# Kernel optimization log

Measured on AMD Instinct MI355X. Metric: run time of the kernel, lower is better.

The kernel has to match this reference:

```python
import jax, jax.numpy as jnp
import numpy as np

EPS = 1e-5  # BatchNorm1d default eps


def setup_inputs() -> dict:
    key = jax.random.key(0)
    ks = jax.random.split(key, 8)
    B, N, C = 4, 4096, 512
    Ci = C // 2
    s = 1.0 / np.sqrt(C)
    si = 1.0 / np.sqrt(Ci)
    return {
        "x": jax.random.normal(ks[0], (B, N, C), jnp.float32),
        "gamma": jnp.ones((C,), jnp.float32),
        "beta": jnp.zeros((C,), jnp.float32),
        "theta_w": jax.random.normal(ks[1], (Ci, C), jnp.float32) * s,
        "theta_b": jnp.zeros((Ci,), jnp.float32),
        "phi_w": jax.random.normal(ks[2], (Ci, C), jnp.float32) * s,
        "phi_b": jnp.zeros((Ci,), jnp.float32),
        "g_w": jax.random.normal(ks[3], (Ci, C), jnp.float32) * s,
        "g_b": jnp.zeros((Ci,), jnp.float32),
        "w_w": jax.random.normal(ks[4], (C, Ci), jnp.float32) * si,
        "w_b": jnp.zeros((C,), jnp.float32),
    }


def reference(x, gamma, beta, theta_w, theta_b, phi_w, phi_b, g_w, g_b, w_w, w_b):
    # x: (B, N, C). BatchNorm1d in training mode: stats over batch and length dims.
    mean = jnp.mean(x, axis=(0, 1))                     # (C,)
    var = jnp.mean((x - mean) ** 2, axis=(0, 1))        # biased variance, (C,)
    feat = jax.nn.relu(gamma * (x - mean) * jax.lax.rsqrt(var + EPS) + beta)

    t = jnp.einsum('bnc,dc->bnd', feat, theta_w) + theta_b   # (B, N, Ci)
    p = jnp.einsum('bnc,dc->bnd', feat, phi_w) + phi_b       # (B, N, Ci)
    gx = jnp.einsum('bnc,dc->bnd', feat, g_w) + g_b          # (B, N, Ci)

    attn = jnp.einsum('bqd,bkd->bqk', t, p)             # unscaled QK^T, (B, N, N)
    attn = jax.nn.softmax(attn, axis=-1)
    y = jnp.einsum('bqk,bkd->bqd', attn, gx)            # (B, N, Ci)

    w_y = jnp.einsum('bnd,cd->bnc', y, w_w) + w_b       # (B, N, C)
    return x + w_y
```

## Files before the change

### kernel.cpp

```cpp
#include <hip/hip_runtime.h>

typedef unsigned short u16;
typedef __attribute__((ext_vector_type(4))) float f32x4;
typedef __attribute__((ext_vector_type(8))) _Float16 f16x8;
typedef __attribute__((ext_vector_type(8))) unsigned short u16x8;
typedef __attribute__((ext_vector_type(4))) unsigned short u16x4;

#define DEV __device__ __forceinline__

DEV u16 f2h(float f) {
    _Float16 h = (_Float16)f;
    u16 r;
    __builtin_memcpy(&r, &h, 2);
    return r;
}
DEV float h2f(u16 u) {
    _Float16 h;
    __builtin_memcpy(&h, &u, 2);
    return (float)h;
}

DEV f32x4 mfma16(f16x8 a, f16x8 b, f32x4 c) {
    return __builtin_amdgcn_mfma_f32_16x16x32_f16(a, b, c, 0, 0, 0);
}

DEV void gload16(const void* g, void* l) {
    __builtin_amdgcn_global_load_lds(
        (const __attribute__((address_space(1))) void*)g,
        (__attribute__((address_space(3))) void*)l, 16, 0, 0);
}

#define BB 4
#define NN 4096
#define CC 512
#define CI 256
#define RR (BB * NN)

#define OFF_FEAT 0u
#define OFF_Q    16777216u
#define OFF_K    25165824u
#define OFF_V    33554432u
#define OFF_Y    41943040u
#define OFF_WQKV 50331648u
#define OFF_WO   51118080u
#define OFF_BQKV 51380224u
#define OFF_PART 51383296u
#define OFF_SS   51907584u

__global__ void bn_partial(const float* __restrict__ x, float* __restrict__ part) {
    const int c = threadIdx.x;
    const int blk = blockIdx.x;
    const float* xp = x + (size_t)blk * 128 * CC + c;
    float s = 0.f, q = 0.f;
    for (int r = 0; r < 128; r++) {
        float v = xp[(size_t)r * CC];
        s += v; q += v * v;
    }
    part[blk * 1024 + c] = s;
    part[blk * 1024 + 512 + c] = q;
}

__global__ void bn_final(const float* __restrict__ part,
                         const float* __restrict__ gamma, const float* __restrict__ beta,
                         float* __restrict__ ss) {
    const int c = threadIdx.x;
    float s = 0.f, q = 0.f;
    for (int i = 0; i < 128; i++) {
        s += part[i * 1024 + c];
        q += part[i * 1024 + 512 + c];
    }
    float m = s * (1.0f / (float)RR);
    float var = q * (1.0f / (float)RR) - m * m;
    float istd = rsqrtf(var + 1e-5f);
    float g = gamma[c] * istd;
    ss[c] = g;
    ss[512 + c] = beta[c] - m * g;
}

__global__ void cvt_weights(const float* __restrict__ thw, const float* __restrict__ phw,
                            const float* __restrict__ gw,
                            const float* __restrict__ thb, const float* __restrict__ phb,
                            const float* __restrict__ gb,
                            const float* __restrict__ ww,
                            u16* __restrict__ wqkv, u16* __restrict__ wo,
                            float* __restrict__ bqkv) {
    const int idx = blockIdx.x * 256 + threadIdx.x;
    if (idx < 768 * 512) {
        int row = idx >> 9, col = idx & 511;
        float v = (row < 256) ? thw[row * 512 + col]
                : (row < 512) ? phw[(row - 256) * 512 + col]
                              : gw[(row - 512) * 512 + col];
        wqkv[idx] = f2h(v);
    } else if (idx < 768 * 512 + 512 * 256) {
        int j = idx - 768 * 512;
        wo[j] = f2h(ww[j]);
    }
    if (idx < 768) {
        bqkv[idx] = (idx < 256) ? thb[idx] : (idx < 512) ? phb[idx - 256] : gb[idx - 512];
    }
}

__global__ void feat_kernel(const float* __restrict__ x, const float* __restrict__ ss,
                            u16* __restrict__ feat) {
    const int total = RR * CC / 4;
    for (int idx = blockIdx.x * blockDim.x + threadIdx.x; idx < total;
         idx += gridDim.x * blockDim.x) {
        f32x4 xv = ((const f32x4*)x)[idx];
        int c4 = idx & 127;
        f32x4 sc = ((const f32x4*)ss)[c4];
        f32x4 sh = ((const f32x4*)(ss + 512))[c4];
        u16x4 o;
        #pragma unroll
        for (int e = 0; e < 4; e++) {
            float f = fmaxf(xv[e] * sc[e] + sh[e], 0.f);
            o[e] = f2h(f);
        }
        ((u16x4*)feat)[idx] = o;
    }
}

template <int MODE>
__global__ __launch_bounds__(256) void gemm_bt(
    const u16* __restrict__ A, const u16* __restrict__ Bm, int K,
    const float* __restrict__ bias, const float* __restrict__ xres,
    u16* __restrict__ oq, u16* __restrict__ okk, u16* __restrict__ ov,
    float* __restrict__ of) {
    __shared__ u16 As[128 * 32];
    __shared__ u16 Bs[128 * 32];
    const int tid = threadIdx.x;
    const int lane = tid & 63;
    const int l15 = lane & 15, kg = lane >> 4;
    const int wv = tid >> 6;
    const int wm = wv >> 1, wn = wv & 1;
    const int m0 = blockIdx.x * 128, n0 = blockIdx.y * 128;

    f32x4 acc[4][4];
    #pragma unroll
    for (int i = 0; i < 4; i++)
        #pragma unroll
        for (int j = 0; j < 4; j++) acc[i][j] = (f32x4){0.f, 0.f, 0.f, 0.f};

    const int rowA = tid >> 2, colA = (tid & 3) * 8;
    for (int k0 = 0; k0 < K; k0 += 32) {
        gload16(A + (size_t)(m0 + rowA) * K + k0 + colA, &As[tid * 8]);
        gload16(A + (size_t)(m0 + 64 + rowA) * K + k0 + colA, &As[2048 + tid * 8]);
        gload16(Bm + (size_t)(n0 + rowA) * K + k0 + colA, &Bs[tid * 8]);
        gload16(Bm + (size_t)(n0 + 64 + rowA) * K + k0 + colA, &Bs[2048 + tid * 8]);
        __syncthreads();
        f16x8 af[4], bfr[4];
        #pragma unroll
        for (int i = 0; i < 4; i++)
            af[i] = *(const f16x8*)&As[(wm * 64 + i * 16 + l15) * 32 + kg * 8];
        #pragma unroll
        for (int i = 0; i < 4; i++)
            bfr[i] = *(const f16x8*)&Bs[(wn * 64 + i * 16 + l15) * 32 + kg * 8];
        #pragma unroll
        for (int mi = 0; mi < 4; mi++)
            #pragma unroll
            for (int ni = 0; ni < 4; ni++)
                acc[mi][ni] = mfma16(af[mi], bfr[ni], acc[mi][ni]);
        __syncthreads();
    }

    #pragma unroll
    for (int mi = 0; mi < 4; mi++) {
        #pragma unroll
        for (int ni = 0; ni < 4; ni++) {
            #pragma unroll
            for (int r = 0; r < 4; r++) {
                int row = m0 + wm * 64 + mi * 16 + kg * 4 + r;
                int col = n0 + wn * 64 + ni * 16 + l15;
                float v = acc[mi][ni][r];
                if constexpr (MODE == 0) {
                    v += bias[col];
                    u16 hv = f2h(v);
                    if (n0 < 256) {
                        oq[(size_t)row * CI + col] = hv;
                    } else if (n0 < 512) {
                        okk[(size_t)row * CI + (col - 256)] = hv;
                    } else {
                        int d = col - 512;
                        int bi = row >> 12, key = row & (NN - 1);
                        int k5 = key & 31;
                        int skey = (key & ~31) |
                                   ((((k5 >> 2) & 3) << 3) | (k5 & 3) | (((k5 >> 4) & 1) << 2));
                        ov[((size_t)bi * CI + d) * NN + skey] = hv;
                    }
                } else {
                    size_t o = (size_t)row * 512 + col;
                    of[o] = xres[o] + v + bias[col];
                }
            }
        }
    }
}

#define KVB 32
#define NSPLIT 4
#define KEYS_PER (NN / NSPLIT)
#define NTILE (KEYS_PER / KVB)
#define ATTN_LDS 65536

DEV void stageK32(const u16* __restrict__ Kg, size_t kvbase, int kv0, u16* Ks, int tid) {
    const int chunk = tid & 31, rb = tid >> 5;
    #pragma unroll
    for (int i = 0; i < 4; i++) {
        int row = i * 8 + rb;
        int sc = chunk ^ (row & 7);
        gload16(Kg + kvbase + (size_t)(kv0 + row) * CI + sc * 8,
                &Ks[row * 256 + chunk * 8]);
    }
}

DEV void stageV32(const u16* __restrict__ Vtg, size_t vbase, int kv0, u16* Vt, int tid) {
    const int c = tid & 3, db = tid >> 2;
    #pragma unroll
    for (int i = 0; i < 4; i++) {
        int d = i * 64 + db;
        int sc = c ^ ((d >> 1) & 3);
        gload16(Vtg + vbase + (size_t)d * NN + kv0 + sc * 8,
                &Vt[d * KVB + c * 8]);
    }
}

__global__ __launch_bounds__(256, 2) void attn_kernel(
    const u16* __restrict__ Qg, const u16* __restrict__ Kg,
    const u16* __restrict__ Vtg, u16* __restrict__ po01, u16* __restrict__ po23,
    float* __restrict__ ml) {
    extern __shared__ u16 smem[];

    const int tid = threadIdx.x, lane = tid & 63, wv = tid >> 6;
    const int l15 = lane & 15, kg = lane >> 4;
    const int sid = (blockIdx.x & 7) * 64 + (blockIdx.x >> 3);
    const int qt = sid & 31;
    const int b = (sid >> 5) & 3;
    const int sp = sid >> 7;
    const int kvoff = sp * KEYS_PER;
    const size_t kvbase = (size_t)b * NN * CI;
    const size_t vbase = (size_t)b * CI * NN;

    f16x8 qf[2][8];
    {
        const u16* qp0 = Qg + ((size_t)b * NN + qt * 128 + wv * 32 + l15) * CI + kg * 8;
        #pragma unroll
        for (int qs = 0; qs < 2; qs++)
            #pragma unroll
            for (int kk = 0; kk < 8; kk++)
                qf[qs][kk] = *(const f16x8*)(qp0 + (size_t)qs * 16 * CI + kk * 32);
    }

    f32x4 acc[16][2];
    #pragma unroll
    for (int i = 0; i < 16; i++)
        #pragma unroll
        for (int qs = 0; qs < 2; qs++) acc[i][qs] = (f32x4){0.f, 0.f, 0.f, 0.f};
    float mrow[2] = {-1e30f, -1e30f}, lrow[2] = {0.f, 0.f};

    stageK32(Kg, kvbase, kvoff, smem, tid);
    stageV32(Vtg, vbase, kvoff, smem + 16384, tid);
    __syncthreads();

    for (int it = 0; it < NTILE; ++it) {
        const u16* Ks = smem + (it & 1) * 8192;
        const u16* Vt = smem + 16384 + (it & 1) * 8192;
        if (it + 1 < NTILE) {
            const int nxt = ((it + 1) & 1) * 8192;
            stageK32(Kg, kvbase, kvoff + (it + 1) * KVB, smem + nxt, tid);
            stageV32(Vtg, vbase, kvoff + (it + 1) * KVB, smem + 16384 + nxt, tid);
        }

        f32x4 s[2][2];
        #pragma unroll
        for (int qs = 0; qs < 2; qs++)
            #pragma unroll
            for (int nt = 0; nt < 2; nt++) s[qs][nt] = (f32x4){0.f, 0.f, 0.f, 0.f};
        __builtin_amdgcn_s_setprio(1);
        #pragma unroll
        for (int kk = 0; kk < 8; kk++) {
            #pragma unroll
            for (int nt = 0; nt < 2; nt++) {
                int krow = nt * 16 + l15;
                f16x8 kf = *(const f16x8*)&Ks[krow * 256 + (((kk * 4 + kg) ^ (krow & 7)) << 3)];
                s[0][nt] = mfma16(kf, qf[0][kk], s[0][nt]);
                s[1][nt] = mfma16(kf, qf[1][kk], s[1][nt]);
            }
        }
        __builtin_amdgcn_s_setprio(0);

        float mx[2];
        #pragma unroll
        for (int qs = 0; qs < 2; qs++) {
            float m8 = fmaxf(fmaxf(fmaxf(s[qs][0][0], s[qs][0][1]), fmaxf(s[qs][0][2], s[qs][0][3])),
                             fmaxf(fmaxf(s[qs][1][0], s[qs][1][1]), fmaxf(s[qs][1][2], s[qs][1][3])));
            m8 = fmaxf(m8, __shfl_xor(m8, 16));
            m8 = fmaxf(m8, __shfl_xor(m8, 32));
            mx[qs] = m8;
        }
        float need = fmaxf(mx[0] - mrow[0], mx[1] - mrow[1]);
        if (!__all(need <= 8.f)) {
            float sclv[2];
            #pragma unroll
            for (int qs = 0; qs < 2; qs++) {
                float mnew = fmaxf(mrow[qs], mx[qs]);
                sclv[qs] = __expf(mrow[qs] - mnew);
                lrow[qs] *= sclv[qs];
                mrow[qs] = mnew;
            }
            #pragma unroll
            for (int qs = 0; qs < 2; qs++)
                #pragma unroll
                for (int r = 0; r < 4; r++) {
                    float sr = __shfl(sclv[qs], (lane & 48) | (kg * 4 + r), 64);
                    #pragma unroll
                    for (int dt = 0; dt < 16; dt++) acc[dt][qs][r] *= sr;
                }
        }
        f16x8 pa[2];
        #pragma unroll
        for (int qs = 0; qs < 2; qs++) {
            float rs = 0.f;
            #pragma unroll
            for (int nt = 0; nt < 2; nt++)
                #pragma unroll
                for (int r = 0; r < 4; r++) {
                    float p = __expf(s[qs][nt][r] - mrow[qs]);
                    rs += p;
                    pa[qs][nt * 4 + r] = (_Float16)p;
                }
            rs += __shfl_xor(rs, 16);
            rs += __shfl_xor(rs, 32);
            lrow[qs] += rs;
        }

        __builtin_amdgcn_s_setprio(1);
        #pragma unroll
        for (int dt = 0; dt < 16; dt++) {
            int d = dt * 16 + l15;
            f16x8 vf = *(const f16x8*)&Vt[d * KVB + ((kg ^ ((l15 >> 1) & 3)) << 3)];
            acc[dt][0] = mfma16(pa[0], vf, acc[dt][0]);
            acc[dt][1] = mfma16(pa[1], vf, acc[dt][1]);
        }
        __builtin_amdgcn_s_setprio(0);

        __syncthreads();
    }

    const int row0 = b * NN + qt * 128 + wv * 32;
    u16* pod = (sp < 2) ? (po01 + (size_t)sp * RR * CI)
                        : (po23 + (size_t)(sp - 2) * RR * CI);
    #pragma unroll
    for (int qs = 0; qs < 2; qs++)
        #pragma unroll
        for (int r = 0; r < 4; r++) {
            float li = __shfl(lrow[qs], (lane & 48) | (kg * 4 + r), 64);
            float inv = 1.f / li;
            int row = row0 + qs * 16 + kg * 4 + r;
            #pragma unroll
            for (int dt = 0; dt < 16; dt++)
                pod[(size_t)row * CI + dt * 16 + l15] = f2h(acc[dt][qs][r] * inv);
        }
    if (kg == 0) {
        #pragma unroll
        for (int qs = 0; qs < 2; qs++) {
            int row = row0 + qs * 16 + l15;
            ml[row * 8 + sp * 2] = mrow[qs];
            ml[row * 8 + sp * 2 + 1] = lrow[qs];
        }
    }
}

__global__ void attn_combine(const u16* __restrict__ po01, const u16* __restrict__ po23,
                             const float* __restrict__ ml, u16* __restrict__ yb) {
    const int gid = blockIdx.x * 256 + threadIdx.x;
    const int row = gid >> 6;
    const int d0 = (gid & 63) * 4;
    f32x4 ml0 = ((const f32x4*)ml)[row * 2];
    f32x4 ml1 = ((const f32x4*)ml)[row * 2 + 1];
    float m = fmaxf(fmaxf(ml0[0], ml0[2]), fmaxf(ml1[0], ml1[2]));
    float c0 = __expf(ml0[0] - m) * ml0[1];
    float c1 = __expf(ml0[2] - m) * ml0[3];
    float c2 = __expf(ml1[0] - m) * ml1[1];
    float c3 = __expf(ml1[2] - m) * ml1[3];
    float inv = 1.f / (c0 + c1 + c2 + c3);
    u16x4 p0 = *(const u16x4*)(po01 + (size_t)row * CI + d0);
    u16x4 p1 = *(const u16x4*)(po01 + (size_t)RR * CI + (size_t)row * CI + d0);
    u16x4 p2 = *(const u16x4*)(po23 + (size_t)row * CI + d0);
    u16x4 p3 = *(const u16x4*)(po23 + (size_t)RR * CI + (size_t)row * CI + d0);
    u16x4 o;
    #pragma unroll
    for (int e = 0; e < 4; e++)
        o[e] = f2h((c0 * h2f(p0[e]) + c1 * h2f(p1[e]) +
                    c2 * h2f(p2[e]) + c3 * h2f(p3[e])) * inv);
    *(u16x4*)(yb + (size_t)row * CI + d0) = o;
}

extern "C" void kernel_launch(void* const* d_in, const int* in_sizes, int n_in,
                              void* d_out, int out_size, void* d_ws, size_t ws_size,
                              hipStream_t stream) {
    (void)in_sizes; (void)n_in; (void)out_size; (void)ws_size;
    const float* x     = (const float*)d_in[0];
    const float* gamma = (const float*)d_in[1];
    const float* beta  = (const float*)d_in[2];
    const float* thw   = (const float*)d_in[3];
    const float* thb   = (const float*)d_in[4];
    const float* phw   = (const float*)d_in[5];
    const float* phb   = (const float*)d_in[6];
    const float* gw    = (const float*)d_in[7];
    const float* gb    = (const float*)d_in[8];
    const float* ww    = (const float*)d_in[9];
    const float* wb    = (const float*)d_in[10];

    char* ws = (char*)d_ws;
    u16* feat  = (u16*)(ws + OFF_FEAT);
    u16* qb    = (u16*)(ws + OFF_Q);
    u16* kb    = (u16*)(ws + OFF_K);
    u16* vtb   = (u16*)(ws + OFF_V);
    u16* yb    = (u16*)(ws + OFF_Y);
    u16* wqkv  = (u16*)(ws + OFF_WQKV);
    u16* wo    = (u16*)(ws + OFF_WO);
    float* bqkv = (float*)(ws + OFF_BQKV);
    float* part = (float*)(ws + OFF_PART);
    float* ss   = (float*)(ws + OFF_SS);
    float* out  = (float*)d_out;
    u16* po23  = (u16*)d_out;

    (void)hipFuncSetAttribute((const void*)attn_kernel,
                              hipFuncAttributeMaxDynamicSharedMemorySize, ATTN_LDS);

    bn_partial<<<128, 512, 0, stream>>>(x, part);
    bn_final<<<1, 512, 0, stream>>>(part, gamma, beta, ss);
    cvt_weights<<<2048, 256, 0, stream>>>(thw, phw, gw, thb, phb, gb, ww, wqkv, wo, bqkv);
    feat_kernel<<<2048, 256, 0, stream>>>(x, ss, feat);
    gemm_bt<0><<<dim3(128, 6), 256, 0, stream>>>(feat, wqkv, 512, bqkv, nullptr,
                                                 qb, kb, vtb, nullptr);
    attn_kernel<<<512, 256, ATTN_LDS, stream>>>(qb, kb, vtb, feat, po23, part);
    attn_combine<<<RR * CI / 4 / 256, 256, 0, stream>>>(feat, po23, part, yb);
    gemm_bt<1><<<dim3(128, 4), 256, 0, stream>>>(yb, wo, 256, wb, x,
                                                 nullptr, nullptr, nullptr, out);
}
```

Baseline: 163.1 us.

## Split attention keys six ways and single-buffer K to fit three blocks per CU

The attention kernel now splits the key range into six uneven chunks instead of four, launching 768 blocks, and raises launch bounds to three blocks per CU. To fit that occupancy, K staging drops double buffering: K is reloaded into one LDS buffer after an extra barrier following the QK product, while V stays double buffered, cutting LDS from 64 KB to 48 KB. The partial outputs and softmax stats are relocated across the output buffer, the feat buffer and the weight workspace, and the combine kernel merges six partials. The trade-off is an added barrier and exposed K load latency per tile, plus more partial-output traffic in the combine step, in exchange for more resident waves and better CU fill.

```diff
diff --git a/kernel.cpp b/kernel.cpp
--- a/kernel.cpp
+++ b/kernel.cpp
@@ -196,10 +196,8 @@
 }
 
 #define KVB 32
-#define NSPLIT 4
-#define KEYS_PER (NN / NSPLIT)
-#define NTILE (KEYS_PER / KVB)
-#define ATTN_LDS 65536
+#define NSPLIT 6
+#define ATTN_LDS 49152
 
 DEV void stageK32(const u16* __restrict__ Kg, size_t kvbase, int kv0, u16* Ks, int tid) {
     const int chunk = tid & 31, rb = tid >> 5;
@@ -223,19 +221,21 @@
     }
 }
 
-__global__ __launch_bounds__(256, 2) void attn_kernel(
+__global__ __launch_bounds__(256, 3) void attn_kernel(
     const u16* __restrict__ Qg, const u16* __restrict__ Kg,
-    const u16* __restrict__ Vtg, u16* __restrict__ po01, u16* __restrict__ po23,
+    const u16* __restrict__ Vtg, u16* __restrict__ poA, u16* __restrict__ poB,
     float* __restrict__ ml) {
     extern __shared__ u16 smem[];
 
     const int tid = threadIdx.x, lane = tid & 63, wv = tid >> 6;
     const int l15 = lane & 15, kg = lane >> 4;
-    const int sid = (blockIdx.x & 7) * 64 + (blockIdx.x >> 3);
+    const int sid = (blockIdx.x & 7) * 96 + (blockIdx.x >> 3);
     const int qt = sid & 31;
     const int b = (sid >> 5) & 3;
     const int sp = sid >> 7;
-    const int kvoff = sp * KEYS_PER;
+    const int k0 = ((sp * 64) / 3) * 32;
+    const int k1 = (((sp + 1) * 64) / 3) * 32;
+    const int ntile = (k1 - k0) >> 5;
     const size_t kvbase = (size_t)b * NN * CI;
     const size_t vbase = (size_t)b * CI * NN;
 
@@ -256,18 +256,16 @@
         for (int qs = 0; qs < 2; qs++) acc[i][qs] = (f32x4){0.f, 0.f, 0.f, 0.f};
     float mrow[2] = {-1e30f, -1e30f}, lrow[2] = {0.f, 0.f};
 
-    stageK32(Kg, kvbase, kvoff, smem, tid);
-    stageV32(Vtg, vbase, kvoff, smem + 16384, tid);
+    u16* Ks = smem;
+
+    stageK32(Kg, kvbase, k0, Ks, tid);
+    stageV32(Vtg, vbase, k0, smem + 8192, tid);
     __syncthreads();
 
-    for (int it = 0; it < NTILE; ++it) {
-        const u16* Ks = smem + (it & 1) * 8192;
-        const u16* Vt = smem + 16384 + (it & 1) * 8192;
-        if (it + 1 < NTILE) {
-            const int nxt = ((it + 1) & 1) * 8192;
-            stageK32(Kg, kvbase, kvoff + (it + 1) * KVB, smem + nxt, tid);
-            stageV32(Vtg, vbase, kvoff + (it + 1) * KVB, smem + 16384 + nxt, tid);
-        }
+    for (int it = 0; it < ntile; ++it) {
+        const u16* Vt = smem + 8192 + (it & 1) * 8192;
+        if (it + 1 < ntile)
+            stageV32(Vtg, vbase, k0 + (it + 1) * KVB, smem + 8192 + (((it + 1) & 1) * 8192), tid);
 
         f32x4 s[2][2];
         #pragma unroll
@@ -286,6 +284,10 @@
             }
         }
         __builtin_amdgcn_s_setprio(0);
+
+        __syncthreads();
+        if (it + 1 < ntile)
+            stageK32(Kg, kvbase, k0 + (it + 1) * KVB, Ks, tid);
 
         float mx[2];
         #pragma unroll
@@ -346,8 +348,8 @@
     }
 
     const int row0 = b * NN + qt * 128 + wv * 32;
-    u16* pod = (sp < 2) ? (po01 + (size_t)sp * RR * CI)
-                        : (po23 + (size_t)(sp - 2) * RR * CI);
+    u16* pod = (sp < 4) ? (poA + (size_t)sp * RR * CI)
+                        : (poB + (size_t)(sp - 4) * RR * CI);
     #pragma unroll
     for (int qs = 0; qs < 2; qs++)
         #pragma unroll
@@ -363,35 +365,43 @@
         #pragma unroll
         for (int qs = 0; qs < 2; qs++) {
             int row = row0 + qs * 16 + l15;
-            ml[row * 8 + sp * 2] = mrow[qs];
-            ml[row * 8 + sp * 2 + 1] = lrow[qs];
-        }
-    }
-}
-
-__global__ void attn_combine(const u16* __restrict__ po01, const u16* __restrict__ po23,
+            ml[row * 12 + sp * 2] = mrow[qs];
+            ml[row * 12 + sp * 2 + 1] = lrow[qs];
+        }
+    }
+}
+
+__global__ void attn_combine(const u16* __restrict__ poA, const u16* __restrict__ poB,
                              const float* __restrict__ ml, u16* __restrict__ yb) {
     const int gid = blockIdx.x * 256 + threadIdx.x;
     const int row = gid >> 6;
     const int d0 = (gid & 63) * 4;
-    f32x4 ml0 = ((const f32x4*)ml)[row * 2];
-    f32x4 ml1 = ((const f32x4*)ml)[row * 2 + 1];
-    float m = fmaxf(fmaxf(ml0[0], ml0[2]), fmaxf(ml1[0], ml1[2]));
+    f32x4 ml0 = ((const f32x4*)ml)[row * 3];
+    f32x4 ml1 = ((const f32x4*)ml)[row * 3 + 1];
+    f32x4 ml2 = ((const f32x4*)ml)[row * 3 + 2];
+    float m = fmaxf(fmaxf(fmaxf(ml0[0], ml0[2]), fmaxf(ml1[0], ml1[2])),
+                    fmaxf(ml2[0], ml2[2]));
     float c0 = __expf(ml0[0] - m) * ml0[1];
     float c1 = __expf(ml0[2] - m) * ml0[3];
     float c2 = __expf(ml1[0] - m) * ml1[1];
     float c3 = __expf(ml1[2] - m) * ml1[3];
-    float inv = 1.f / (c0 + c1 + c2 + c3);
-    u16x4 p0 = *(const u16x4*)(po01 + (size_t)row * CI + d0);
-    u16x4 p1 = *(const u16x4*)(po01 + (size_t)RR * CI + (size_t)row * CI + d0);
-    u16x4 p2 = *(const u16x4*)(po23 + (size_t)row * CI + d0);
-    u16x4 p3 = *(const u16x4*)(po23 + (size_t)RR * CI + (size_t)row * CI + d0);
+    float c4 = __expf(ml2[0] - m) * ml2[1];
+    float c5 = __expf(ml2[2] - m) * ml2[3];
+    float inv = 1.f / (c0 + c1 + c2 + c3 + c4 + c5);
+    const size_t off = (size_t)row * CI + d0;
+    const size_t spstride = (size_t)RR * CI;
+    u16x4 p0 = *(const u16x4*)(poA + off);
+    u16x4 p1 = *(const u16x4*)(poA + spstride + off);
+    u16x4 p2 = *(const u16x4*)(poA + 2 * spstride + off);
+    u16x4 p3 = *(const u16x4*)(poA + 3 * spstride + off);
+    u16x4 p4 = *(const u16x4*)(poB + off);
+    u16x4 p5 = *(const u16x4*)(poB + spstride + off);
     u16x4 o;
     #pragma unroll
     for (int e = 0; e < 4; e++)
-        o[e] = f2h((c0 * h2f(p0[e]) + c1 * h2f(p1[e]) +
-                    c2 * h2f(p2[e]) + c3 * h2f(p3[e])) * inv);
-    *(u16x4*)(yb + (size_t)row * CI + d0) = o;
+        o[e] = f2h((c0 * h2f(p0[e]) + c1 * h2f(p1[e]) + c2 * h2f(p2[e]) +
+                    c3 * h2f(p3[e]) + c4 * h2f(p4[e]) + c5 * h2f(p5[e])) * inv);
+    *(u16x4*)(yb + off) = o;
 }
 
 extern "C" void kernel_launch(void* const* d_in, const int* in_sizes, int n_in,
@@ -422,7 +432,8 @@
     float* part = (float*)(ws + OFF_PART);
     float* ss   = (float*)(ws + OFF_SS);
     float* out  = (float*)d_out;
-    u16* po23  = (u16*)d_out;
+    u16* poA   = (u16*)d_out;
+    float* mlp = (float*)(ws + OFF_WQKV);
 
     (void)hipFuncSetAttribute((const void*)attn_kernel,
                               hipFuncAttributeMaxDynamicSharedMemorySize, ATTN_LDS);
@@ -433,8 +444,8 @@
     feat_kernel<<<2048, 256, 0, stream>>>(x, ss, feat);
     gemm_bt<0><<<dim3(128, 6), 256, 0, stream>>>(feat, wqkv, 512, bqkv, nullptr,
                                                  qb, kb, vtb, nullptr);
-    attn_kernel<<<512, 256, ATTN_LDS, stream>>>(qb, kb, vtb, feat, po23, part);
-    attn_combine<<<RR * CI / 4 / 256, 256, 0, stream>>>(feat, po23, part, yb);
+    attn_kernel<<<768, 256, ATTN_LDS, stream>>>(qb, kb, vtb, poA, feat, mlp);
+    attn_combine<<<RR * CI / 4 / 256, 256, 0, stream>>>(poA, feat, mlp, yb);
     gemm_bt<1><<<dim3(128, 4), 256, 0, stream>>>(yb, wo, 256, wb, x,
                                                  nullptr, nullptr, nullptr, out);
 }
```

Result: slower. 366.6 us (+124.7%).
